# Kernel tuning notes

Measured on AMD Instinct MI355X. Metric: run time of the kernel, lower is better.

## Reference

```python
import jax, jax.numpy as jnp
import numpy as np

NUM_HEADS = 8
NEG_INF = -1e30


def _within_bucket_rank(idx):
    # idx: [U] int32 bucket ids; returns occurrence count of each id among earlier positions
    U = idx.shape[0]
    order = jnp.argsort(idx, stable=True)
    sv = idx[order]
    pos = jnp.arange(U, dtype=jnp.int32)
    is_start = jnp.concatenate([jnp.ones((1,), bool), sv[1:] != sv[:-1]])
    start = jax.lax.cummax(jnp.where(is_start, pos, 0))
    rank = pos - start
    return jnp.zeros(U, jnp.int32).at[order].set(rank)


def setup_inputs() -> dict:
    key = jax.random.key(0)
    ks = jax.random.split(key, 10)
    B, U, G, E = 8, 16384, 64, 128
    lin = jnp.linspace(0.0, 1.0, G)
    gx, gy = jnp.meshgrid(lin, lin, indexing='ij')
    xc_on_grid = jnp.broadcast_to(jnp.stack([gx, gy], -1), (B, G, G, 2)).astype(jnp.float32)
    s = 0.02
    return {
        'xc_off_grid': jax.random.uniform(ks[0], (B, U, 2), jnp.float32),
        'xc_on_grid': xc_on_grid,
        'zc_off_grid': jax.random.normal(ks[1], (B, U, E), jnp.float32),
        'zc_on_grid': jax.random.normal(ks[2], (B, G, G, E), jnp.float32),
        'latents': jax.random.normal(ks[3], (G * G, E), jnp.float32),
        'fake_embedding': jax.random.normal(ks[4], (E,), jnp.float32),
        'Wq': jax.random.normal(ks[5], (E, E), jnp.float32) * s,
        'Wk': jax.random.normal(ks[6], (E, E), jnp.float32) * s,
        'Wv': jax.random.normal(ks[7], (E, E), jnp.float32) * s,
        'Wo': jax.random.normal(ks[8], (E, E), jnp.float32) * s,
        'ignore_on_grid': 0,
    }


def _bucketize(xc_off_grid, xc_on_grid):
    # returns nearest flat grid index per off-grid point, shape [B, U] int32
    B = xc_off_grid.shape[0]
    dims = xc_on_grid.shape[1:-1]
    S = int(np.prod(dims))
    grid_shape = jnp.asarray(dims, jnp.float32)
    x_on = xc_on_grid.reshape(B, S, -1)
    xmin = x_on.min(axis=(0, 1))
    xmax = x_on.max(axis=(0, 1))
    spacing = (xmax - xmin) / (grid_shape - 1.0)
    nm = jnp.floor((xc_off_grid - xmin + spacing / 2) / spacing)
    nm = jnp.clip(nm, 0.0, grid_shape - 1.0)
    # strides as in the original: flip(cumprod([1, *dims])[:-1])
    strides = np.flip(np.cumprod(np.concatenate([[1], np.asarray(dims)]))[:-1]).astype(np.float32)
    return (nm * jnp.asarray(strides)).sum(-1).astype(jnp.int32)


def _mhca(latents_q, kv, valid, Wq, Wk, Wv, Wo):
    # latents_q: [N,1,E], kv: [N,P,E], valid: [N,P] bool
    N, P, E = kv.shape
    H, Dh = NUM_HEADS, E // NUM_HEADS
    q = (latents_q @ Wq).reshape(N, 1, H, Dh)
    k = (kv @ Wk).reshape(N, P, H, Dh)
    v = (kv @ Wv).reshape(N, P, H, Dh)
    scores = jnp.einsum('nqhd,nkhd->nhqk', q, k) / jnp.sqrt(jnp.asarray(Dh, q.dtype))
    scores = jnp.where(valid[:, None, None, :], scores, NEG_INF)
    attn = jax.nn.softmax(scores, axis=-1)
    out = jnp.einsum('nhqk,nkhd->nqhd', attn, v).reshape(N, 1, E)
    return out @ Wo


def reference(xc_off_grid, xc_on_grid, zc_off_grid, zc_on_grid, latents, fake_embedding, Wq, Wk, Wv, Wo, ignore_on_grid):
    B, U, E = zc_off_grid.shape
    dims = xc_on_grid.shape[1:-1]
    S = int(np.prod(dims))
    z_on = zc_on_grid.reshape(B, S, E)

    nearest_idx = _bucketize(xc_off_grid, xc_on_grid)          # [B, U]
    cumcount = jax.vmap(_within_bucket_rank)(nearest_idx)       # [B, U]
    flat_seg = (nearest_idx + jnp.arange(B, dtype=jnp.int32)[:, None] * S).reshape(-1)
    counts = jax.ops.segment_sum(jnp.ones(B * U, jnp.int32), flat_seg, num_segments=B * S)
    max_patch = int(jax.device_get(counts.max())) + 1           # +1 slot for on-grid/fake token

    # ragged scatter of off-grid tokens into padded per-bucket buffer
    grid_stacked = jnp.zeros((B * S, max_patch, E), zc_off_grid.dtype)
    grid_stacked = grid_stacked.at[flat_seg, cumcount.reshape(-1)].set(zc_off_grid.reshape(B * U, E))
    if ignore_on_grid:
        last = jnp.broadcast_to(fake_embedding, (B * S, E))
    else:
        last = z_on.reshape(B * S, E)
    grid_stacked = grid_stacked.at[:, -1].set(last)

    slot = jnp.arange(max_patch)
    valid = (slot[None, :] < counts[:, None]) | (slot[None, :] == max_patch - 1)  # [B*S, P]

    lat = jnp.broadcast_to(latents[None], (B, S, E)).reshape(B * S, 1, E)
    zc = _mhca(lat, grid_stacked, valid, Wq, Wk, Wv, Wo)        # [B*S, 1, E]
    return zc.reshape(B, *dims, E)
```

## Files before the change

kernel.cpp:

```cpp
#include <hip/hip_runtime.h>
#include <hip/hip_bf16.h>
#include <math.h>

namespace {
constexpr int B_  = 8;
constexpr int U_  = 16384;
constexpr int S_  = 4096;
constexpr int E_  = 128;
constexpr int NTOK  = B_ * U_;
constexpr int NCELL = B_ * S_;
constexpr int FUSED_GRID = 1024;
constexpr int CAP = 32;
constexpr int SWZ2 = 2 * 16384;
}

typedef __attribute__((ext_vector_type(8))) short bf16x8;
typedef __attribute__((ext_vector_type(4))) float f32x4;

__device__ inline unsigned short bf16rne(float x) {
  unsigned u = __float_as_uint(x);
  u = u + 0x7fffu + ((u >> 16) & 1u);
  return (unsigned short)(u >> 16);
}

__device__ inline bf16x8 pack8(float4 a, float4 b) {
  union { __hip_bfloat162 h; unsigned int u; } q0, q1, q2, q3;
  q0.h = __float22bfloat162_rn(make_float2(a.x, a.y));
  q1.h = __float22bfloat162_rn(make_float2(a.z, a.w));
  q2.h = __float22bfloat162_rn(make_float2(b.x, b.y));
  q3.h = __float22bfloat162_rn(make_float2(b.z, b.w));
  union { unsigned int u[4]; bf16x8 v; } r;
  r.u[0] = q0.u; r.u[1] = q1.u; r.u[2] = q2.u; r.u[3] = q3.u;
  return r.v;
}

__global__ __launch_bounds__(1024, 4) void setup_kernel(
    const float* __restrict__ Wq, const float* __restrict__ Wk,
    const float* __restrict__ Wv, const float* __restrict__ Wo,
    const float* __restrict__ latents, const float* __restrict__ xc_off,
    unsigned short* __restrict__ Wsw, unsigned short* __restrict__ QKt,
    int* __restrict__ cnt, int* __restrict__ sorted) {
  const int tid = threadIdx.x;

  if (blockIdx.x < 128) {
    __shared__ __align__(16) unsigned short wq[16384];
    __shared__ float wkt[128 * 129];
    __shared__ float qbuf[32 * 128];
    const int s0 = blockIdx.x * 32;

    for (int i = tid; i < 16384; i += 1024) {
      const int k = i >> 7, n = i & 127;
      wq[(((k >> 3) * 128 + n) << 3) + (k & 7)] = bf16rne(Wq[i]);
      wkt[(i & 127) * 129 + (i >> 7)] = Wk[i];
    }
    __syncthreads();

    const int wave = tid >> 6, lane = tid & 63;
    const int c = lane & 15, g = lane >> 4;
    if (wave < 2) {
      const int t0w = s0 + wave * 16;
      f32x4 acc[8];
#pragma unroll
      for (int i = 0; i < 8; ++i) acc[i] = {0.f, 0.f, 0.f, 0.f};
      const float* arow = latents + (size_t)(t0w + c) * E_ + g * 8;
      const bf16x8* bq = (const bf16x8*)wq;
#pragma unroll
      for (int ks = 0; ks < 4; ++ks) {
        float4 a0 = *(const float4*)(arow + ks * 32);
        float4 a1 = *(const float4*)(arow + ks * 32 + 4);
        bf16x8 af = pack8(a0, a1);
        const int bo = (ks * 4 + g) * 128 + c;
#pragma unroll
        for (int nt = 0; nt < 8; ++nt)
          acc[nt] = __builtin_amdgcn_mfma_f32_16x16x32_bf16(af, bq[bo + nt * 16], acc[nt], 0, 0, 0);
      }
#pragma unroll
      for (int nt = 0; nt < 8; ++nt)
#pragma unroll
        for (int r = 0; r < 4; ++r)
          qbuf[(wave * 16 + g * 4 + r) * 128 + nt * 16 + c] = acc[nt][r] * 0.25f;
    }
    __syncthreads();

#pragma unroll
    for (int k = 0; k < 32; ++k) {
      const int o = k * 1024 + tid;
      const int e = o & 127, h = (o >> 7) & 7, sl = o >> 10;
      float acc = 0.f;
#pragma unroll
      for (int j = 0; j < 16; ++j)
        acc = fmaf(wkt[(h * 16 + j) * 129 + e], qbuf[sl * 128 + h * 16 + j], acc);
      QKt[(size_t)(s0 + sl) * 1024 + (e >> 3) * 64 + h * 8 + (e & 7)] = bf16rne(acc);
    }
  } else {
    const int base = (blockIdx.x - 128) * 1024 + tid;
    const int stride = 128 * 1024;
    for (int i = base; i < SWZ2 + NTOK; i += stride) {
      if (i < SWZ2) {
        const int w = i >> 14, e = i & 16383;
        const int k = e >> 7, n = e & 127;
        const float* src = (w == 0) ? Wv : Wo;
        Wsw[w * 16384 + (((k >> 3) * 128 + n) << 3) + (k & 7)] = bf16rne(src[e]);
      } else {
        const int tok = i - SWZ2;
        const int b = tok >> 14;
        const float sp = 1.0f / 63.0f;
        const float half = sp * 0.5f;
        const float x0 = xc_off[(size_t)tok * 2 + 0];
        const float x1 = xc_off[(size_t)tok * 2 + 1];
        float n0 = floorf((x0 - 0.0f + half) / sp);
        float n1 = floorf((x1 - 0.0f + half) / sp);
        n0 = fminf(fmaxf(n0, 0.0f), 63.0f);
        n1 = fminf(fmaxf(n1, 0.0f), 63.0f);
        const int seg = b * S_ + (int)(n0 * 64.0f + n1);
        const int rank = atomicAdd(&cnt[seg], 1);
        if (rank < CAP) sorted[seg * CAP + rank] = tok;
      }
    }
  }
}

__global__ __launch_bounds__(512, 4) void fused_cells(
    const float* __restrict__ zc_off, const float* __restrict__ zc_on,
    const float* __restrict__ fake, const int* __restrict__ ignore_flag,
    const unsigned short* __restrict__ Wv_sw,
    const unsigned short* __restrict__ QKt, const int* __restrict__ cnt,
    const int* __restrict__ sorted, float* __restrict__ out) {
  __shared__ __align__(16) unsigned short wv[16384];
  __shared__ float wbuf[8][16][9];
  const int tid = threadIdx.x;
  {
    const uint4* sv = (const uint4*)Wv_sw;
    uint4* dv = (uint4*)wv;
#pragma unroll
    for (int i = 0; i < 4; ++i) dv[i * 512 + tid] = sv[i * 512 + tid];
  }
  const int ign = *ignore_flag;
  __syncthreads();

  const int wave = tid >> 6, lane = tid & 63;
  const int c = lane & 15, g = lane >> 4;
  const int half = c >> 3;
  const int hwr  = g >> 1;
  const bf16x8* bv = (const bf16x8*)wv;

  for (int grp = blockIdx.x; grp < NCELL / 16; grp += FUSED_GRID) {
    const int slot = grp * 8 + wave;
    const int cA = slot * 2, cB = cA + 1;
    const int sA = cA & (S_ - 1);
    const int nA = min(cnt[cA], CAP);
    const int nB = min(cnt[cB], CAP);
    const int cH = half ? cB : cA;
    const int nH = half ? nB : nA;
    const int baseH = cH * CAP;
    const bf16x8* bqk = (const bf16x8*)(QKt + (size_t)(sA + half) * 1024);

    float num_acc[8], den_acc[8];
#pragma unroll
    for (int i = 0; i < 8; ++i) { num_acc[i] = 0.f; den_acc[i] = 0.f; }

    const int chunks = max((nA + 8) >> 3, (nB + 8) >> 3);

    for (int ch = 0; ch < chunks; ++ch) {
      const int jj = ch * 8 + (c & 7);
      const float* arow;
      if (jj < nH)       arow = zc_off + (size_t)sorted[baseH + jj] * E_;
      else if (jj == nH) arow = ign ? fake : (zc_on + (size_t)cH * E_);
      else               arow = zc_on;
      arow += g * 8;

      bf16x8 af[4];
#pragma unroll
      for (int ks = 0; ks < 4; ++ks) {
        float4 a0 = *(const float4*)(arow + ks * 32);
        float4 a1 = *(const float4*)(arow + ks * 32 + 4);
        af[ks] = pack8(a0, a1);
      }

      f32x4 aS = {0.f, 0.f, 0.f, 0.f};
#pragma unroll
      for (int ks = 0; ks < 4; ++ks)
        aS = __builtin_amdgcn_mfma_f32_16x16x32_bf16(af[ks], bqk[(ks * 4 + g) * 8 + (c & 7)], aS, 0, 0, 0);

      if (hwr == half) {
#pragma unroll
        for (int r = 0; r < 4; ++r) {
          const int t = g * 4 + r;
          const int jt = ch * 8 + (t & 7);
          wbuf[wave][t][c & 7] = (jt <= nH) ? __expf(aS[r]) : 0.f;
        }
      }

#pragma unroll 2
      for (int h = 0; h < 8; ++h) {
        float wr[4];
#pragma unroll
        for (int r = 0; r < 4; ++r) wr[r] = wbuf[wave][g * 4 + r][h];

        const int bo = g * 128 + c + h * 16;
        f32x4 aV = {0.f, 0.f, 0.f, 0.f};
#pragma unroll
        for (int ks = 0; ks < 4; ++ks)
          aV = __builtin_amdgcn_mfma_f32_16x16x32_bf16(af[ks], bv[bo + ks * 512], aV, 0, 0, 0);

        float sv = 0.f, sd = 0.f;
#pragma unroll
        for (int r = 0; r < 4; ++r) { sv = fmaf(wr[r], aV[r], sv); sd += wr[r]; }
        num_acc[h] += sv;
        den_acc[h] += sd;
      }
    }

#pragma unroll
    for (int i = 0; i < 8; ++i) {
      num_acc[i] += __shfl_xor(num_acc[i], 16, 64);
      den_acc[i] += __shfl_xor(den_acc[i], 16, 64);
    }
    const int cellO = hwr ? cB : cA;
    const int hb = (g & 1) * 4;
#pragma unroll
    for (int b = 0; b < 4; ++b) {
      const int h = hb + b;
      out[(size_t)cellO * E_ + h * 16 + c] = num_acc[h] / den_acc[h];
    }
  }
}

__global__ __launch_bounds__(512, 4) void finalize_mfma(
    const unsigned short* __restrict__ Wo_sw, float* __restrict__ out) {
  __shared__ __align__(16) unsigned short wo[16384];
  const int tid = threadIdx.x;
  {
    const uint4* s = (const uint4*)Wo_sw;
    uint4* d = (uint4*)wo;
#pragma unroll
    for (int i = 0; i < 4; ++i) d[i * 512 + tid] = s[i * 512 + tid];
  }
  __syncthreads();

  const int wave = tid >> 6, lane = tid & 63;
  const int c = lane & 15, g = lane >> 4;
  const int t0w = blockIdx.x * 128 + wave * 16;

  f32x4 acc[8];
#pragma unroll
  for (int i = 0; i < 8; ++i) acc[i] = {0.f, 0.f, 0.f, 0.f};

  const float* nrow = out + (size_t)(t0w + c) * E_ + g * 8;
  const bf16x8* bo_ = (const bf16x8*)wo;
#pragma unroll
  for (int ks = 0; ks < 4; ++ks) {
    float4 a0 = *(const float4*)(nrow + ks * 32);
    float4 a1 = *(const float4*)(nrow + ks * 32 + 4);
    bf16x8 af = pack8(a0, a1);
    const int bofs = (ks * 4 + g) * 128 + c;
#pragma unroll
    for (int nt = 0; nt < 8; ++nt)
      acc[nt] = __builtin_amdgcn_mfma_f32_16x16x32_bf16(af, bo_[bofs + nt * 16], acc[nt], 0, 0, 0);
  }
#pragma unroll
  for (int nt = 0; nt < 8; ++nt)
#pragma unroll
    for (int r = 0; r < 4; ++r)
      out[(size_t)(t0w + g * 4 + r) * E_ + nt * 16 + c] = acc[nt][r];
}

extern "C" void kernel_launch(void* const* d_in, const int* in_sizes, int n_in,
                              void* d_out, int out_size, void* d_ws, size_t ws_size,
                              hipStream_t stream) {
  const float* xc_off  = (const float*)d_in[0];
  const float* zc_off  = (const float*)d_in[2];
  const float* zc_on   = (const float*)d_in[3];
  const float* latents = (const float*)d_in[4];
  const float* fake    = (const float*)d_in[5];
  const float* Wq      = (const float*)d_in[6];
  const float* Wk      = (const float*)d_in[7];
  const float* Wv      = (const float*)d_in[8];
  const float* Wo      = (const float*)d_in[9];
  const int*   ignore  = (const int*)d_in[10];

  float* out = (float*)d_out;

  unsigned short* QKt = (unsigned short*)d_ws;
  unsigned short* Wsw = QKt + (size_t)S_ * 1024;
  int* cnt    = (int*)(Wsw + SWZ2);
  int* sorted = cnt + NCELL;
  unsigned short* Wv_sw = Wsw;
  unsigned short* Wo_sw = Wsw + 16384;

  hipMemsetAsync(cnt, 0, NCELL * sizeof(int), stream);
  setup_kernel<<<256, 1024, 0, stream>>>(Wq, Wk, Wv, Wo, latents, xc_off,
                                         Wsw, QKt, cnt, sorted);
  fused_cells<<<FUSED_GRID, 512, 0, stream>>>(zc_off, zc_on, fake, ignore,
                                              Wv_sw, QKt, cnt, sorted, out);
  finalize_mfma<<<NCELL / 128, 512, 0, stream>>>(Wo_sw, out);
}
```

Baseline: 177.2 us.

## Precompute Wq·Wkᵀ product and compute QKt via separate split-bf16 MFMA GEMM

Reassociates the per-latent key projection: first forms the per-head product A = Wq_h·Wk_hᵀ (scaled) once in setup, stored as hi/lo bf16 pairs, then a new qkt_gemm kernel computes latents·A with MFMA over 256 blocks. This replaces the old per-block LDS transpose plus scalar FMA loop that dominated setup blocks. The fused_cells kernel also drops its grid-stride loop and launches one block per 16-cell group. It adds an extra kernel launch and workspace for the A matrices, and the hi/lo split doubles MFMA count to preserve precision.

```diff
diff --git a/kernel.cpp b/kernel.cpp
--- a/kernel.cpp
+++ b/kernel.cpp
@@ -9,9 +9,9 @@
 constexpr int E_  = 128;
 constexpr int NTOK  = B_ * U_;
 constexpr int NCELL = B_ * S_;
-constexpr int FUSED_GRID = 1024;
 constexpr int CAP = 32;
 constexpr int SWZ2 = 2 * 16384;
+constexpr int ASZ  = 128 * 1024;
 }
 
 typedef __attribute__((ext_vector_type(8))) short bf16x8;
@@ -21,6 +21,10 @@
   unsigned u = __float_as_uint(x);
   u = u + 0x7fffu + ((u >> 16) & 1u);
   return (unsigned short)(u >> 16);
+}
+
+__device__ inline float bf16tof(unsigned short h) {
+  return __uint_as_float(((unsigned)h) << 16);
 }
 
 __device__ inline bf16x8 pack8(float4 a, float4 b) {
@@ -37,64 +41,48 @@
 __global__ __launch_bounds__(1024, 4) void setup_kernel(
     const float* __restrict__ Wq, const float* __restrict__ Wk,
     const float* __restrict__ Wv, const float* __restrict__ Wo,
-    const float* __restrict__ latents, const float* __restrict__ xc_off,
-    unsigned short* __restrict__ Wsw, unsigned short* __restrict__ QKt,
+    const float* __restrict__ xc_off,
+    unsigned short* __restrict__ Wsw,
+    unsigned short* __restrict__ Ahi, unsigned short* __restrict__ Alo,
     int* __restrict__ cnt, int* __restrict__ sorted) {
   const int tid = threadIdx.x;
 
-  if (blockIdx.x < 128) {
-    __shared__ __align__(16) unsigned short wq[16384];
-    __shared__ float wkt[128 * 129];
-    __shared__ float qbuf[32 * 128];
-    const int s0 = blockIdx.x * 32;
-
-    for (int i = tid; i < 16384; i += 1024) {
-      const int k = i >> 7, n = i & 127;
-      wq[(((k >> 3) * 128 + n) << 3) + (k & 7)] = bf16rne(Wq[i]);
-      wkt[(i & 127) * 129 + (i >> 7)] = Wk[i];
-    }
-    __syncthreads();
-
-    const int wave = tid >> 6, lane = tid & 63;
-    const int c = lane & 15, g = lane >> 4;
-    if (wave < 2) {
-      const int t0w = s0 + wave * 16;
-      f32x4 acc[8];
-#pragma unroll
-      for (int i = 0; i < 8; ++i) acc[i] = {0.f, 0.f, 0.f, 0.f};
-      const float* arow = latents + (size_t)(t0w + c) * E_ + g * 8;
-      const bf16x8* bq = (const bf16x8*)wq;
-#pragma unroll
-      for (int ks = 0; ks < 4; ++ks) {
-        float4 a0 = *(const float4*)(arow + ks * 32);
-        float4 a1 = *(const float4*)(arow + ks * 32 + 4);
-        bf16x8 af = pack8(a0, a1);
-        const int bo = (ks * 4 + g) * 128 + c;
-#pragma unroll
-        for (int nt = 0; nt < 8; ++nt)
-          acc[nt] = __builtin_amdgcn_mfma_f32_16x16x32_bf16(af, bq[bo + nt * 16], acc[nt], 0, 0, 0);
+  if (blockIdx.x < 16) {
+    const int n = tid;
+    const int eg = n >> 6, h = (n >> 3) & 7, el = n & 7;
+    const int e = eg * 8 + el;
+    const float* wk = Wk + (size_t)e * 128 + h * 16;
+    float wkv[16];
+#pragma unroll
+    for (int j = 0; j < 16; j += 4) {
+      float4 t = *(const float4*)(wk + j);
+      wkv[j] = t.x; wkv[j + 1] = t.y; wkv[j + 2] = t.z; wkv[j + 3] = t.w;
+    }
+    union { unsigned short s[8]; uint4 v; } rh, rl;
+#pragma unroll
+    for (int r = 0; r < 8; ++r) {
+      const int k = (blockIdx.x << 3) + r;
+      const float* wq = Wq + (size_t)k * 128 + h * 16;
+      float acc = 0.f;
+#pragma unroll
+      for (int j = 0; j < 16; j += 4) {
+        float4 t = *(const float4*)(wq + j);
+        acc = fmaf(t.x, wkv[j], acc);
+        acc = fmaf(t.y, wkv[j + 1], acc);
+        acc = fmaf(t.z, wkv[j + 2], acc);
+        acc = fmaf(t.w, wkv[j + 3], acc);
       }
-#pragma unroll
-      for (int nt = 0; nt < 8; ++nt)
-#pragma unroll
-        for (int r = 0; r < 4; ++r)
-          qbuf[(wave * 16 + g * 4 + r) * 128 + nt * 16 + c] = acc[nt][r] * 0.25f;
-    }
-    __syncthreads();
-
-#pragma unroll
-    for (int k = 0; k < 32; ++k) {
-      const int o = k * 1024 + tid;
-      const int e = o & 127, h = (o >> 7) & 7, sl = o >> 10;
-      float acc = 0.f;
-#pragma unroll
-      for (int j = 0; j < 16; ++j)
-        acc = fmaf(wkt[(h * 16 + j) * 129 + e], qbuf[sl * 128 + h * 16 + j], acc);
-      QKt[(size_t)(s0 + sl) * 1024 + (e >> 3) * 64 + h * 8 + (e & 7)] = bf16rne(acc);
-    }
+      acc *= 0.25f;
+      const unsigned short hh = bf16rne(acc);
+      rh.s[r] = hh;
+      rl.s[r] = bf16rne(acc - bf16tof(hh));
+    }
+    const size_t fo = ((size_t)blockIdx.x * 1024 + n) * 8;
+    *(uint4*)(Ahi + fo) = rh.v;
+    *(uint4*)(Alo + fo) = rl.v;
   } else {
-    const int base = (blockIdx.x - 128) * 1024 + tid;
-    const int stride = 128 * 1024;
+    const int base = (blockIdx.x - 16) * 1024 + tid;
+    const int stride = 112 * 1024;
     for (int i = base; i < SWZ2 + NTOK; i += stride) {
       if (i < SWZ2) {
         const int w = i >> 14, e = i & 16383;
@@ -120,6 +108,46 @@
   }
 }
 
+__global__ __launch_bounds__(512, 4) void qkt_gemm(
+    const float* __restrict__ latents,
+    const unsigned short* __restrict__ Ahi,
+    const unsigned short* __restrict__ Alo,
+    unsigned short* __restrict__ QKt) {
+  const int tid = threadIdx.x;
+  const int wave = tid >> 6, lane = tid & 63;
+  const int c = lane & 15, g = lane >> 4;
+  const int rb = blockIdx.x >> 1, cb = blockIdx.x & 1;
+  const int wr = wave >> 2, wc = wave & 3;
+  const int t0 = rb * 32 + wr * 16;
+  const int n0 = cb * 512 + wc * 128;
+
+  f32x4 acc[8];
+#pragma unroll
+  for (int i = 0; i < 8; ++i) acc[i] = {0.f, 0.f, 0.f, 0.f};
+
+  const float* arow = latents + (size_t)(t0 + c) * E_ + g * 8;
+#pragma unroll
+  for (int ks = 0; ks < 4; ++ks) {
+    float4 a0 = *(const float4*)(arow + ks * 32);
+    float4 a1 = *(const float4*)(arow + ks * 32 + 4);
+    bf16x8 af = pack8(a0, a1);
+    const size_t kg = (size_t)(ks * 4 + g) * 1024;
+#pragma unroll
+    for (int nt = 0; nt < 8; ++nt) {
+      const size_t fo = (kg + n0 + nt * 16 + c) * 8;
+      acc[nt] = __builtin_amdgcn_mfma_f32_16x16x32_bf16(
+          af, *(const bf16x8*)(Ahi + fo), acc[nt], 0, 0, 0);
+      acc[nt] = __builtin_amdgcn_mfma_f32_16x16x32_bf16(
+          af, *(const bf16x8*)(Alo + fo), acc[nt], 0, 0, 0);
+    }
+  }
+#pragma unroll
+  for (int nt = 0; nt < 8; ++nt)
+#pragma unroll
+    for (int r = 0; r < 4; ++r)
+      QKt[(size_t)(t0 + g * 4 + r) * 1024 + n0 + nt * 16 + c] = bf16rne(acc[nt][r]);
+}
+
 __global__ __launch_bounds__(512, 4) void fused_cells(
     const float* __restrict__ zc_off, const float* __restrict__ zc_on,
     const float* __restrict__ fake, const int* __restrict__ ignore_flag,
@@ -144,85 +172,83 @@
   const int hwr  = g >> 1;
   const bf16x8* bv = (const bf16x8*)wv;
 
-  for (int grp = blockIdx.x; grp < NCELL / 16; grp += FUSED_GRID) {
-    const int slot = grp * 8 + wave;
-    const int cA = slot * 2, cB = cA + 1;
-    const int sA = cA & (S_ - 1);
-    const int nA = min(cnt[cA], CAP);
-    const int nB = min(cnt[cB], CAP);
-    const int cH = half ? cB : cA;
-    const int nH = half ? nB : nA;
-    const int baseH = cH * CAP;
-    const bf16x8* bqk = (const bf16x8*)(QKt + (size_t)(sA + half) * 1024);
-
-    float num_acc[8], den_acc[8];
-#pragma unroll
-    for (int i = 0; i < 8; ++i) { num_acc[i] = 0.f; den_acc[i] = 0.f; }
-
-    const int chunks = max((nA + 8) >> 3, (nB + 8) >> 3);
-
-    for (int ch = 0; ch < chunks; ++ch) {
-      const int jj = ch * 8 + (c & 7);
-      const float* arow;
-      if (jj < nH)       arow = zc_off + (size_t)sorted[baseH + jj] * E_;
-      else if (jj == nH) arow = ign ? fake : (zc_on + (size_t)cH * E_);
-      else               arow = zc_on;
-      arow += g * 8;
-
-      bf16x8 af[4];
-#pragma unroll
-      for (int ks = 0; ks < 4; ++ks) {
-        float4 a0 = *(const float4*)(arow + ks * 32);
-        float4 a1 = *(const float4*)(arow + ks * 32 + 4);
-        af[ks] = pack8(a0, a1);
+  const int slot = blockIdx.x * 8 + wave;
+  const int cA = slot * 2, cB = cA + 1;
+  const int sA = cA & (S_ - 1);
+  const int nA = min(cnt[cA], CAP);
+  const int nB = min(cnt[cB], CAP);
+  const int cH = half ? cB : cA;
+  const int nH = half ? nB : nA;
+  const int baseH = cH * CAP;
+  const bf16x8* bqk = (const bf16x8*)(QKt + (size_t)(sA + half) * 1024);
+
+  float num_acc[8], den_acc[8];
+#pragma unroll
+  for (int i = 0; i < 8; ++i) { num_acc[i] = 0.f; den_acc[i] = 0.f; }
+
+  const int chunks = max((nA + 8) >> 3, (nB + 8) >> 3);
+
+  for (int ch = 0; ch < chunks; ++ch) {
+    const int jj = ch * 8 + (c & 7);
+    const float* arow;
+    if (jj < nH)       arow = zc_off + (size_t)sorted[baseH + jj] * E_;
+    else if (jj == nH) arow = ign ? fake : (zc_on + (size_t)cH * E_);
+    else               arow = zc_on;
+    arow += g * 8;
+
+    bf16x8 af[4];
+#pragma unroll
+    for (int ks = 0; ks < 4; ++ks) {
+      float4 a0 = *(const float4*)(arow + ks * 32);
+      float4 a1 = *(const float4*)(arow + ks * 32 + 4);
+      af[ks] = pack8(a0, a1);
+    }
+
+    f32x4 aS = {0.f, 0.f, 0.f, 0.f};
+#pragma unroll
+    for (int ks = 0; ks < 4; ++ks)
+      aS = __builtin_amdgcn_mfma_f32_16x16x32_bf16(af[ks], bqk[(ks * 4 + g) * 8 + (c & 7)], aS, 0, 0, 0);
+
+    if (hwr == half) {
+#pragma unroll
+      for (int r = 0; r < 4; ++r) {
+        const int t = g * 4 + r;
+        const int jt = ch * 8 + (t & 7);
+        wbuf[wave][t][c & 7] = (jt <= nH) ? __expf(aS[r]) : 0.f;
       }
-
-      f32x4 aS = {0.f, 0.f, 0.f, 0.f};
+    }
+
+#pragma unroll 2
+    for (int h = 0; h < 8; ++h) {
+      float wr[4];
+#pragma unroll
+      for (int r = 0; r < 4; ++r) wr[r] = wbuf[wave][g * 4 + r][h];
+
+      const int bo = g * 128 + c + h * 16;
+      f32x4 aV = {0.f, 0.f, 0.f, 0.f};
 #pragma unroll
       for (int ks = 0; ks < 4; ++ks)
-        aS = __builtin_amdgcn_mfma_f32_16x16x32_bf16(af[ks], bqk[(ks * 4 + g) * 8 + (c & 7)], aS, 0, 0, 0);
-
-      if (hwr == half) {
-#pragma unroll
-        for (int r = 0; r < 4; ++r) {
-          const int t = g * 4 + r;
-          const int jt = ch * 8 + (t & 7);
-          wbuf[wave][t][c & 7] = (jt <= nH) ? __expf(aS[r]) : 0.f;
-        }
-      }
-
-#pragma unroll 2
-      for (int h = 0; h < 8; ++h) {
-        float wr[4];
-#pragma unroll
-        for (int r = 0; r < 4; ++r) wr[r] = wbuf[wave][g * 4 + r][h];
-
-        const int bo = g * 128 + c + h * 16;
-        f32x4 aV = {0.f, 0.f, 0.f, 0.f};
-#pragma unroll
-        for (int ks = 0; ks < 4; ++ks)
-          aV = __builtin_amdgcn_mfma_f32_16x16x32_bf16(af[ks], bv[bo + ks * 512], aV, 0, 0, 0);
-
-        float sv = 0.f, sd = 0.f;
-#pragma unroll
-        for (int r = 0; r < 4; ++r) { sv = fmaf(wr[r], aV[r], sv); sd += wr[r]; }
-        num_acc[h] += sv;
-        den_acc[h] += sd;
-      }
-    }
-
-#pragma unroll
-    for (int i = 0; i < 8; ++i) {
-      num_acc[i] += __shfl_xor(num_acc[i], 16, 64);
-      den_acc[i] += __shfl_xor(den_acc[i], 16, 64);
-    }
-    const int cellO = hwr ? cB : cA;
-    const int hb = (g & 1) * 4;
-#pragma unroll
-    for (int b = 0; b < 4; ++b) {
-      const int h = hb + b;
-      out[(size_t)cellO * E_ + h * 16 + c] = num_acc[h] / den_acc[h];
-    }
+        aV = __builtin_amdgcn_mfma_f32_16x16x32_bf16(af[ks], bv[bo + ks * 512], aV, 0, 0, 0);
+
+      float sv = 0.f, sd = 0.f;
+#pragma unroll
+      for (int r = 0; r < 4; ++r) { sv = fmaf(wr[r], aV[r], sv); sd += wr[r]; }
+      num_acc[h] += sv;
+      den_acc[h] += sd;
+    }
+  }
+
+#pragma unroll
+  for (int i = 0; i < 8; ++i) {
+    num_acc[i] += __shfl_xor(num_acc[i], 16, 64);
+    den_acc[i] += __shfl_xor(den_acc[i], 16, 64);
+  }
+  const int cellO = hwr ? cB : cA;
+  const int hb = (g & 1) * 4;
+#pragma unroll
+  for (int b = 0; b < 4; ++b) {
+    const int h = hb + b;
+    out[(size_t)cellO * E_ + h * 16 + c] = num_acc[h] / den_acc[h];
   }
 }
 
@@ -285,13 +311,16 @@
   unsigned short* Wsw = QKt + (size_t)S_ * 1024;
   int* cnt    = (int*)(Wsw + SWZ2);
   int* sorted = cnt + NCELL;
+  unsigned short* Ahi = (unsigned short*)(sorted + NCELL * CAP);
+  unsigned short* Alo = Ahi + ASZ;
   unsigned short* Wv_sw = Wsw;
   unsigned short* Wo_sw = Wsw + 16384;
 
   hipMemsetAsync(cnt, 0, NCELL * sizeof(int), stream);
-  setup_kernel<<<256, 1024, 0, stream>>>(Wq, Wk, Wv, Wo, latents, xc_off,
-                                         Wsw, QKt, cnt, sorted);
-  fused_cells<<<FUSED_GRID, 512, 0, stream>>>(zc_off, zc_on, fake, ignore,
-                                              Wv_sw, QKt, cnt, sorted, out);
+  setup_kernel<<<128, 1024, 0, stream>>>(Wq, Wk, Wv, Wo, xc_off,
+                                         Wsw, Ahi, Alo, cnt, sorted);
+  qkt_gemm<<<256, 512, 0, stream>>>(latents, Ahi, Alo, QKt);
+  fused_cells<<<2048, 512, 0, stream>>>(zc_off, zc_on, fake, ignore,
+                                        Wv_sw, QKt, cnt, sorted, out);
   finalize_mfma<<<NCELL / 128, 512, 0, stream>>>(Wo_sw, out);
 }
```

After: 191.4 us. 1.08x slower.
